# Performance work log

Measured on AMD Instinct MI355X. Metric: run time of the kernel, lower is better.

The kernel has to match this reference:

```python
import jax, jax.numpy as jnp
import numpy as np

B, N, DIN, DMID, DOUT, E = 64, 5000, 64, 128, 32, 80000


def setup_inputs() -> dict:
    key = jax.random.key(0)
    ks = jax.random.split(key, 12)
    p = lambda k, shape: jax.random.normal(k, shape, jnp.float32) * 0.05
    return {
        "x": jax.random.normal(ks[0], (B, N, DIN), jnp.float32),
        "edge_index": jax.random.randint(ks[1], (2, E), 0, N),
        "prev_hidden_state": jax.random.normal(ks[2], (B, N, DMID), jnp.float32),
        # GCNConv weights/biases for gates z, r, h
        "Wg_z": p(ks[3], (DIN, DMID)), "bg_z": jnp.zeros((DMID,), jnp.float32),
        "Wg_r": p(ks[4], (DIN, DMID)), "bg_r": jnp.zeros((DMID,), jnp.float32),
        "Wg_h": p(ks[5], (DIN, DMID)), "bg_h": jnp.zeros((DMID,), jnp.float32),
        # gate Linear layers on concat([conv_out, H]) -> DMID
        "Wl_z": p(ks[6], (2 * DMID, DMID)), "bl_z": jnp.zeros((DMID,), jnp.float32),
        "Wl_r": p(ks[7], (2 * DMID, DMID)), "bl_r": jnp.zeros((DMID,), jnp.float32),
        "Wl_h": p(ks[8], (2 * DMID, DMID)), "bl_h": jnp.zeros((DMID,), jnp.float32),
        # final output Linear
        "W_out": p(ks[9], (DMID, DOUT)), "b_out": jnp.zeros((DOUT,), jnp.float32),
    }


def reference(x, edge_index, prev_hidden_state,
              Wg_z, bg_z, Wg_r, bg_r, Wg_h, bg_h,
              Wl_z, bl_z, Wl_r, bl_r, Wl_h, bl_h,
              W_out, b_out):
    # GCN symmetric normalization with self-loops (pyg gcn_norm, improved=False)
    row, col = edge_index[0], edge_index[1]
    loop = jnp.arange(N)
    src = jnp.concatenate([row, loop])          # [E+N]
    dst = jnp.concatenate([col, loop])          # [E+N]
    ew = jnp.ones((E + N,), x.dtype)
    deg = jnp.zeros((N,), x.dtype).at[dst].add(ew)
    dis = jnp.where(deg > 0, jax.lax.rsqrt(jnp.maximum(deg, 1e-12)), 0.0)
    norm = dis[src] * ew * dis[dst]             # [E+N]

    def gcn(w, b):
        xw = jnp.einsum('bnd,de->bne', x, w)            # [B,N,DMID]
        msg = xw[:, src, :] * norm[None, :, None]       # gather + weight
        out = jnp.zeros((B, N, w.shape[1]), x.dtype).at[:, dst, :].add(msg)
        return out + b

    H = prev_hidden_state
    Z = jax.nn.sigmoid(jnp.concatenate([gcn(Wg_z, bg_z), H], -1) @ Wl_z + bl_z)
    R = jax.nn.sigmoid(jnp.concatenate([gcn(Wg_r, bg_r), H], -1) @ Wl_r + bl_r)
    Ht = jnp.tanh(jnp.concatenate([gcn(Wg_h, bg_h), H * R], -1) @ Wl_h + bl_h)
    H_new = Z * H + (1.0 - Z) * Ht                      # [B,N,DMID]

    y = jnp.mean(H_new, axis=1)                         # MeanAggregation over nodes
    y = jax.nn.relu(y) @ W_out + b_out                  # [B,DOUT]
    return (y, H_new)
```

## Files before the change

### kernel.cpp

```cpp
#include <hip/hip_runtime.h>
#include <cmath>

namespace {

constexpr int B = 64, N = 5000, DIN = 64, DMID = 128, DOUT = 32, E = 80000;
constexpr int NT = (N + 63) / 64;

typedef unsigned short u16;
typedef __attribute__((ext_vector_type(8))) short short8;
typedef __attribute__((ext_vector_type(4))) float floatx4;

#define MFMA16(a, b, c) __builtin_amdgcn_mfma_f32_16x16x32_bf16((a), (b), (c), 0, 0, 0)

__device__ __forceinline__ u16 f2bf(float f) {
  union { float f; unsigned u; } v; v.f = f;
  unsigned r = v.u + 0x7FFFu + ((v.u >> 16) & 1u);
  return (u16)(r >> 16);
}
__device__ __forceinline__ float bf2f(u16 s) {
  union { unsigned u; float f; } v; v.u = ((unsigned)s) << 16;
  return v.f;
}
__device__ __forceinline__ float sigmoid_fast(float x) {
  return __builtin_amdgcn_rcpf(1.f + __expf(-x));
}
__device__ __forceinline__ float tanh_fast(float x) {
  return fmaf(2.f, __builtin_amdgcn_rcpf(1.f + __expf(-2.f * x)), -1.f);
}


__global__ void count_kernel(const int* __restrict__ ei, int* counts) {
  int e = blockIdx.x * 256 + threadIdx.x;
  if (e < E) atomicAdd(&counts[ei[E + e]], 1);
}

__global__ void scan_kernel(int* counts, int* rowptr, float* dis) {
  __shared__ int sdata[1024];
  const int tid = threadIdx.x;
  constexpr int CH = (N + 1023) / 1024;
  int local[CH], cnt[CH];
  int s = 0;
  for (int i = 0; i < CH; i++) {
    int idx = tid * CH + i;
    int c = (idx < N) ? counts[idx] : 0;
    cnt[i] = c;
    local[i] = s;
    s += c;
  }
  sdata[tid] = s;
  __syncthreads();
  for (int off = 1; off < 1024; off <<= 1) {
    int v = (tid >= off) ? sdata[tid - off] : 0;
    __syncthreads();
    sdata[tid] += v;
    __syncthreads();
  }
  int prev = (tid > 0) ? sdata[tid - 1] : 0;
  for (int i = 0; i < CH; i++) {
    int idx = tid * CH + i;
    if (idx < N) {
      rowptr[idx] = prev + local[i];
      dis[idx] = rsqrtf((float)(cnt[i] + 1));
      counts[idx] = 0;
    }
  }
  if (tid == 1023) rowptr[N] = sdata[1023];
}

__global__ void fill_kernel(const int* __restrict__ ei, const int* __restrict__ rowptr,
                            const float* __restrict__ dis, int* counts,
                            int* csr_src, float* csr_w) {
  int e = blockIdx.x * 256 + threadIdx.x;
  if (e >= E) return;
  int r = ei[e], c = ei[E + e];
  int pos = rowptr[c] + atomicAdd(&counts[c], 1);
  csr_src[pos] = r;
  csr_w[pos] = dis[r] * dis[c];
}


__global__ void pack_kernel(const float* Wgz, const float* Wgr, const float* Wgh,
                            const float* Wlz, const float* Wlr, const float* Wlh,
                            const float* bgz, const float* bgr, const float* bgh,
                            const float* blz, const float* blr, const float* blh,
                            u16* wcB, u16* whB, float* bcAll) {
  int t = blockIdx.x * 256 + threadIdx.x;
  const float* Wg[3] = {Wgz, Wgr, Wgh};
  const float* Wl[3] = {Wlz, Wlr, Wlh};
  const float* bg[3] = {bgz, bgr, bgh};
  const float* bl[3] = {blz, blr, blh};
  if (t < 48 * 64) {
    int chunk = t >> 6, lane = t & 63;
    int q = lane >> 4, lm = lane & 15;
    int g = chunk >> 4, rem = chunk & 15, kt = rem >> 3, nt = rem & 7;
    int n = nt * 16 + lm;
#pragma unroll
    for (int jj = 0; jj < 8; jj++) {
      int k = kt * 32 + q * 8 + jj;
      float acc = 0.f;
      for (int j = 0; j < DMID; j++)
        acc = fmaf(Wg[g][k * DMID + j], Wl[g][j * DMID + n], acc);
      wcB[(size_t)(chunk * 64 + lane) * 8 + jj] = f2bf(acc);
    }
  } else if (t < 48 * 64 + 96 * 64) {
    int t2 = t - 48 * 64;
    int chunk = t2 >> 6, lane = t2 & 63;
    int q = lane >> 4, lm = lane & 15;
    int g = chunk >> 5, rem = chunk & 31, kt = rem >> 3, nt = rem & 7;
    int n = nt * 16 + lm;
#pragma unroll
    for (int jj = 0; jj < 8; jj++) {
      int k = kt * 32 + q * 8 + jj;
      whB[(size_t)t2 * 8 + jj] = f2bf(Wl[g][(DMID + k) * DMID + n]);
    }
  } else {
    int t3 = t - 48 * 64 - 96 * 64;
    if (t3 < 384) {
      int g = t3 >> 7, n = t3 & 127;
      float acc = bl[g][n];
      for (int j = 0; j < DMID; j++)
        acc = fmaf(bg[g][j], Wl[g][j * DMID + n], acc);
      bcAll[t3] = acc;
    }
  }
}


__global__ __launch_bounds__(256) void agg_kernel(
    const float* __restrict__ x, const int* __restrict__ rowptr,
    const int* __restrict__ csr_src, const float* __restrict__ csr_w,
    const float* __restrict__ dis, u16* __restrict__ xs) {
  constexpr int G = B * N / 16;
  const int bid = blockIdx.x;
  const int nb = (bid & 7) * (G >> 3) + (bid >> 3);
  const int sub = threadIdx.x >> 4;
  const int l16 = threadIdx.x & 15;
  const int unit = nb * 16 + sub;
  const int b = unit / N;
  const int n = unit - b * N;
  const float* xb = x + (size_t)b * N * DIN;
  const float d = dis[n];
  float4 v = *(const float4*)(xb + (size_t)n * DIN + l16 * 4);
  const float sw = d * d;
  float ax = v.x * sw, ay = v.y * sw, az = v.z * sw, aw = v.w * sw;
  const int s1 = rowptr[n + 1];
  int p = rowptr[n];
  for (; p + 4 <= s1; p += 4) {
    int i0 = csr_src[p], i1 = csr_src[p + 1], i2 = csr_src[p + 2], i3 = csr_src[p + 3];
    float w0 = csr_w[p], w1 = csr_w[p + 1], w2 = csr_w[p + 2], w3 = csr_w[p + 3];
    float4 a0 = *(const float4*)(xb + (size_t)i0 * DIN + l16 * 4);
    float4 a1 = *(const float4*)(xb + (size_t)i1 * DIN + l16 * 4);
    float4 a2 = *(const float4*)(xb + (size_t)i2 * DIN + l16 * 4);
    float4 a3 = *(const float4*)(xb + (size_t)i3 * DIN + l16 * 4);
    ax = fmaf(a0.x, w0, ax); ay = fmaf(a0.y, w0, ay);
    az = fmaf(a0.z, w0, az); aw = fmaf(a0.w, w0, aw);
    ax = fmaf(a1.x, w1, ax); ay = fmaf(a1.y, w1, ay);
    az = fmaf(a1.z, w1, az); aw = fmaf(a1.w, w1, aw);
    ax = fmaf(a2.x, w2, ax); ay = fmaf(a2.y, w2, ay);
    az = fmaf(a2.z, w2, az); aw = fmaf(a2.w, w2, aw);
    ax = fmaf(a3.x, w3, ax); ay = fmaf(a3.y, w3, ay);
    az = fmaf(a3.z, w3, az); aw = fmaf(a3.w, w3, aw);
  }
  for (; p < s1; p++) {
    int i0 = csr_src[p];
    float w0 = csr_w[p];
    float4 a0 = *(const float4*)(xb + (size_t)i0 * DIN + l16 * 4);
    ax = fmaf(a0.x, w0, ax); ay = fmaf(a0.y, w0, ay);
    az = fmaf(a0.z, w0, az); aw = fmaf(a0.w, w0, aw);
  }
  uint2 o;
  o.x = (unsigned)f2bf(ax) | ((unsigned)f2bf(ay) << 16);
  o.y = (unsigned)f2bf(az) | ((unsigned)f2bf(aw) << 16);
  *(uint2*)(xs + (size_t)unit * DIN + l16 * 4) = o;
}


constexpr int SH = 136;

__global__ __launch_bounds__(256, 4) void fused_mfma(
    const u16* __restrict__ xs, const float* __restrict__ H,
    const u16* __restrict__ wcB, const u16* __restrict__ whB,
    const float* __restrict__ bcAll,
    float* __restrict__ hnew, float* __restrict__ partials) {
  __shared__ u16 H_s[64 * SH];

  const int tid = threadIdx.x;
  const int b = blockIdx.y;
  const int n0 = blockIdx.x * 64;
  const int lane = tid & 63, w = tid >> 6;
  const int q = lane >> 4, lm = lane & 15;
  const int w16 = w * 16;

#pragma unroll
  for (int j = 0; j < 8; j++) {
    int idx = j * 64 + lane;
    int rl = idx >> 5, seg = idx & 31;
    int row = w16 + rl;
    float4 v = make_float4(0.f, 0.f, 0.f, 0.f);
    if (n0 + row < N) v = *(const float4*)(H + ((size_t)b * N + n0 + row) * DMID + seg * 4);
    uint2 p;
    p.x = (unsigned)f2bf(v.x) | ((unsigned)f2bf(v.y) << 16);
    p.y = (unsigned)f2bf(v.z) | ((unsigned)f2bf(v.w) << 16);
    *(uint2*)&H_s[row * SH + seg * 4] = p;
  }

  const int an = n0 + w16 + lm;
  short8 ax[2];
  if (an < N) {
    const u16* xrow = xs + ((size_t)b * N + an) * DIN;
    ax[0] = *(const short8*)(xrow + q * 8);
    ax[1] = *(const short8*)(xrow + 32 + q * 8);
  } else {
    ax[0] = short8{0, 0, 0, 0, 0, 0, 0, 0};
    ax[1] = short8{0, 0, 0, 0, 0, 0, 0, 0};
  }

  short8 ah[4];
#pragma unroll
  for (int kt = 0; kt < 4; kt++)
    ah[kt] = *(const short8*)&H_s[(w16 + lm) * SH + kt * 32 + q * 8];

  uint2 hstash[8];
#pragma unroll
  for (int nt = 0; nt < 8; nt++) {
    floatx4 a = {0.f, 0.f, 0.f, 0.f};
#pragma unroll
    for (int kt = 0; kt < 2; kt++)
      a = MFMA16(ax[kt], *(const short8*)(wcB + (size_t)((16 + kt * 8 + nt) * 64 + lane) * 8), a);
#pragma unroll
    for (int kt = 0; kt < 4; kt++)
      a = MFMA16(ah[kt], *(const short8*)(whB + (size_t)((32 + kt * 8 + nt) * 64 + lane) * 8), a);
    float bias = bcAll[128 + nt * 16 + lm];
    unsigned hx = 0u, hy = 0u;
#pragma unroll
    for (int r = 0; r < 4; r++) {
      int row = w16 + q * 4 + r, col = nt * 16 + lm;
      u16 hb = H_s[row * SH + col];
      float h = bf2f(hb);
      float rg = sigmoid_fast(a[r] + bias);
      H_s[row * SH + col] = f2bf(h * rg);
      if (r < 2) hx |= ((unsigned)hb) << (16 * r);
      else       hy |= ((unsigned)hb) << (16 * (r - 2));
    }
    hstash[nt] = make_uint2(hx, hy);
  }

  floatx4 zpre[8];
#pragma unroll
  for (int nt = 0; nt < 8; nt++) {
    floatx4 a = {0.f, 0.f, 0.f, 0.f};
#pragma unroll
    for (int kt = 0; kt < 2; kt++)
      a = MFMA16(ax[kt], *(const short8*)(wcB + (size_t)((0 + kt * 8 + nt) * 64 + lane) * 8), a);
#pragma unroll
    for (int kt = 0; kt < 4; kt++)
      a = MFMA16(ah[kt], *(const short8*)(whB + (size_t)((0 + kt * 8 + nt) * 64 + lane) * 8), a);
    zpre[nt] = a;
  }

  short8 ahr[4];
#pragma unroll
  for (int kt = 0; kt < 4; kt++)
    ahr[kt] = *(const short8*)&H_s[(w16 + lm) * SH + kt * 32 + q * 8];

#pragma unroll
  for (int nt = 0; nt < 8; nt++) {
    floatx4 ha = {0.f, 0.f, 0.f, 0.f};
#pragma unroll
    for (int kt = 0; kt < 2; kt++)
      ha = MFMA16(ax[kt], *(const short8*)(wcB + (size_t)((32 + kt * 8 + nt) * 64 + lane) * 8), ha);
#pragma unroll
    for (int kt = 0; kt < 4; kt++)
      ha = MFMA16(ahr[kt], *(const short8*)(whB + (size_t)((64 + kt * 8 + nt) * 64 + lane) * 8), ha);
    float zb = bcAll[nt * 16 + lm], hb_ = bcAll[256 + nt * 16 + lm];
    float colsum = 0.f;
#pragma unroll
    for (int r = 0; r < 4; r++) {
      int row = w16 + q * 4 + r;
      bool valid = (n0 + row) < N;
      unsigned word = (r < 2) ? hstash[nt].x : hstash[nt].y;
      float h = bf2f((u16)(word >> (16 * (r & 1))));
      float z = sigmoid_fast(zpre[nt][r] + zb);
      float ht = tanh_fast(ha[r] + hb_);
      float hn = fmaf(z, h - ht, ht);
      if (valid) {
        hnew[((size_t)b * N + n0 + row) * DMID + nt * 16 + lm] = hn;
        colsum += hn;
      }
    }
    colsum += __shfl_xor(colsum, 16);
    colsum += __shfl_xor(colsum, 32);
    if (lane < 16)
      partials[(((size_t)b * NT + blockIdx.x) * 4 + w) * DMID + nt * 16 + lane] = colsum;
  }
}


__global__ void out_kernel(const float* __restrict__ partials, const float* __restrict__ Wout,
                           const float* __restrict__ bout, float* __restrict__ y) {
  const int b = blockIdx.x;
  const int c = threadIdx.x;
  __shared__ float m[DMID];
  float acc = 0.f;
  for (int t = 0; t < NT * 4; t++)
    acc += partials[((size_t)b * NT * 4 + t) * DMID + c];
  m[c] = fmaxf(acc * (1.f / (float)N), 0.f);
  __syncthreads();
  if (c < DOUT) {
    float a2 = bout[c];
    for (int jj = 0; jj < DMID; jj++)
      a2 = fmaf(m[jj], Wout[jj * DOUT + c], a2);
    y[b * DOUT + c] = a2;
  }
}

}

extern "C" void kernel_launch(void* const* d_in, const int* in_sizes, int n_in,
                              void* d_out, int out_size, void* d_ws, size_t ws_size,
                              hipStream_t stream) {
  const float* x = (const float*)d_in[0];
  const int* ei = (const int*)d_in[1];
  const float* H = (const float*)d_in[2];
  const float* Wgz = (const float*)d_in[3];
  const float* bgz = (const float*)d_in[4];
  const float* Wgr = (const float*)d_in[5];
  const float* bgr = (const float*)d_in[6];
  const float* Wgh = (const float*)d_in[7];
  const float* bgh = (const float*)d_in[8];
  const float* Wlz = (const float*)d_in[9];
  const float* blz = (const float*)d_in[10];
  const float* Wlr = (const float*)d_in[11];
  const float* blr = (const float*)d_in[12];
  const float* Wlh = (const float*)d_in[13];
  const float* blh = (const float*)d_in[14];
  const float* Wout = (const float*)d_in[15];
  const float* bout = (const float*)d_in[16];

  float* y = (float*)d_out;
  float* hnew = (float*)d_out + (size_t)B * DOUT;

  char* p = (char*)d_ws;
  auto carve = [&](size_t bytes) {
    char* q = p;
    p += (bytes + 255) & ~size_t(255);
    return q;
  };
  int* counts = (int*)carve((size_t)N * 4);
  int* rowptr = (int*)carve((size_t)(N + 1) * 4);
  int* csr_src = (int*)carve((size_t)E * 4);
  float* csr_w = (float*)carve((size_t)E * 4);
  float* dis = (float*)carve((size_t)N * 4);
  u16* wcB = (u16*)carve((size_t)48 * 64 * 8 * 2);
  u16* whB = (u16*)carve((size_t)96 * 64 * 8 * 2);
  float* bcAll = (float*)carve((size_t)384 * 4);
  float* partials = (float*)carve((size_t)B * NT * 4 * DMID * 4);
  u16* xs = (u16*)carve((size_t)B * N * DIN * 2);

  hipMemsetAsync(counts, 0, (size_t)N * 4, stream);
  pack_kernel<<<38, 256, 0, stream>>>(Wgz, Wgr, Wgh, Wlz, Wlr, Wlh,
                                      bgz, bgr, bgh, blz, blr, blh,
                                      wcB, whB, bcAll);
  count_kernel<<<(E + 255) / 256, 256, 0, stream>>>(ei, counts);
  scan_kernel<<<1, 1024, 0, stream>>>(counts, rowptr, dis);
  fill_kernel<<<(E + 255) / 256, 256, 0, stream>>>(ei, rowptr, dis, counts, csr_src, csr_w);
  agg_kernel<<<B * N / 16, 256, 0, stream>>>(x, rowptr, csr_src, csr_w, dis, xs);
  fused_mfma<<<dim3(NT, B), 256, 0, stream>>>(xs, H, wcB, whB, bcAll, hnew, partials);
  out_kernel<<<B, DMID, 0, stream>>>(partials, Wout, bout, y);
}
```

Measured before the change: 734.4 us.

## Remap aggregation to one block per node across all batches; relax fused launch bounds

```diff
diff --git a/kernel.cpp b/kernel.cpp
--- a/kernel.cpp
+++ b/kernel.cpp
@@ -130,54 +130,75 @@
     const float* __restrict__ x, const int* __restrict__ rowptr,
     const int* __restrict__ csr_src, const float* __restrict__ csr_w,
     const float* __restrict__ dis, u16* __restrict__ xs) {
-  constexpr int G = B * N / 16;
-  const int bid = blockIdx.x;
-  const int nb = (bid & 7) * (G >> 3) + (bid >> 3);
-  const int sub = threadIdx.x >> 4;
-  const int l16 = threadIdx.x & 15;
-  const int unit = nb * 16 + sub;
-  const int b = unit / N;
-  const int n = unit - b * N;
-  const float* xb = x + (size_t)b * N * DIN;
+  const int n = blockIdx.x;
+  const int tb = threadIdx.x >> 2;
+  const int dq = threadIdx.x & 3;
+  const float* xbase = x + (size_t)tb * N * DIN + dq * 16;
+
   const float d = dis[n];
-  float4 v = *(const float4*)(xb + (size_t)n * DIN + l16 * 4);
   const float sw = d * d;
-  float ax = v.x * sw, ay = v.y * sw, az = v.z * sw, aw = v.w * sw;
+  float4 acc[4];
+  {
+    const float4* sp = (const float4*)(xbase + (size_t)n * DIN);
+#pragma unroll
+    for (int i = 0; i < 4; i++) {
+      float4 v = sp[i];
+      acc[i].x = v.x * sw; acc[i].y = v.y * sw;
+      acc[i].z = v.z * sw; acc[i].w = v.w * sw;
+    }
+  }
   const int s1 = rowptr[n + 1];
   int p = rowptr[n];
-  for (; p + 4 <= s1; p += 4) {
-    int i0 = csr_src[p], i1 = csr_src[p + 1], i2 = csr_src[p + 2], i3 = csr_src[p + 3];
-    float w0 = csr_w[p], w1 = csr_w[p + 1], w2 = csr_w[p + 2], w3 = csr_w[p + 3];
-    float4 a0 = *(const float4*)(xb + (size_t)i0 * DIN + l16 * 4);
-    float4 a1 = *(const float4*)(xb + (size_t)i1 * DIN + l16 * 4);
-    float4 a2 = *(const float4*)(xb + (size_t)i2 * DIN + l16 * 4);
-    float4 a3 = *(const float4*)(xb + (size_t)i3 * DIN + l16 * 4);
-    ax = fmaf(a0.x, w0, ax); ay = fmaf(a0.y, w0, ay);
-    az = fmaf(a0.z, w0, az); aw = fmaf(a0.w, w0, aw);
-    ax = fmaf(a1.x, w1, ax); ay = fmaf(a1.y, w1, ay);
-    az = fmaf(a1.z, w1, az); aw = fmaf(a1.w, w1, aw);
-    ax = fmaf(a2.x, w2, ax); ay = fmaf(a2.y, w2, ay);
-    az = fmaf(a2.z, w2, az); aw = fmaf(a2.w, w2, aw);
-    ax = fmaf(a3.x, w3, ax); ay = fmaf(a3.y, w3, ay);
-    az = fmaf(a3.z, w3, az); aw = fmaf(a3.w, w3, aw);
-  }
-  for (; p < s1; p++) {
+  for (; p + 2 <= s1; p += 2) {
+    int i0 = csr_src[p], i1 = csr_src[p + 1];
+    float w0 = csr_w[p], w1 = csr_w[p + 1];
+    const float4* s0p = (const float4*)(xbase + (size_t)i0 * DIN);
+    const float4* s1p = (const float4*)(xbase + (size_t)i1 * DIN);
+    float4 a0[4], a1[4];
+#pragma unroll
+    for (int i = 0; i < 4; i++) a0[i] = s0p[i];
+#pragma unroll
+    for (int i = 0; i < 4; i++) a1[i] = s1p[i];
+#pragma unroll
+    for (int i = 0; i < 4; i++) {
+      acc[i].x = fmaf(a0[i].x, w0, acc[i].x); acc[i].y = fmaf(a0[i].y, w0, acc[i].y);
+      acc[i].z = fmaf(a0[i].z, w0, acc[i].z); acc[i].w = fmaf(a0[i].w, w0, acc[i].w);
+    }
+#pragma unroll
+    for (int i = 0; i < 4; i++) {
+      acc[i].x = fmaf(a1[i].x, w1, acc[i].x); acc[i].y = fmaf(a1[i].y, w1, acc[i].y);
+      acc[i].z = fmaf(a1[i].z, w1, acc[i].z); acc[i].w = fmaf(a1[i].w, w1, acc[i].w);
+    }
+  }
+  if (p < s1) {
     int i0 = csr_src[p];
     float w0 = csr_w[p];
-    float4 a0 = *(const float4*)(xb + (size_t)i0 * DIN + l16 * 4);
-    ax = fmaf(a0.x, w0, ax); ay = fmaf(a0.y, w0, ay);
-    az = fmaf(a0.z, w0, az); aw = fmaf(a0.w, w0, aw);
-  }
-  uint2 o;
-  o.x = (unsigned)f2bf(ax) | ((unsigned)f2bf(ay) << 16);
-  o.y = (unsigned)f2bf(az) | ((unsigned)f2bf(aw) << 16);
-  *(uint2*)(xs + (size_t)unit * DIN + l16 * 4) = o;
+    const float4* s0p = (const float4*)(xbase + (size_t)i0 * DIN);
+#pragma unroll
+    for (int i = 0; i < 4; i++) {
+      float4 v = s0p[i];
+      acc[i].x = fmaf(v.x, w0, acc[i].x); acc[i].y = fmaf(v.y, w0, acc[i].y);
+      acc[i].z = fmaf(v.z, w0, acc[i].z); acc[i].w = fmaf(v.w, w0, acc[i].w);
+    }
+  }
+  uint4 o0, o1;
+  o0.x = (unsigned)f2bf(acc[0].x) | ((unsigned)f2bf(acc[0].y) << 16);
+  o0.y = (unsigned)f2bf(acc[0].z) | ((unsigned)f2bf(acc[0].w) << 16);
+  o0.z = (unsigned)f2bf(acc[1].x) | ((unsigned)f2bf(acc[1].y) << 16);
+  o0.w = (unsigned)f2bf(acc[1].z) | ((unsigned)f2bf(acc[1].w) << 16);
+  o1.x = (unsigned)f2bf(acc[2].x) | ((unsigned)f2bf(acc[2].y) << 16);
+  o1.y = (unsigned)f2bf(acc[2].z) | ((unsigned)f2bf(acc[2].w) << 16);
+  o1.z = (unsigned)f2bf(acc[3].x) | ((unsigned)f2bf(acc[3].y) << 16);
+  o1.w = (unsigned)f2bf(acc[3].z) | ((unsigned)f2bf(acc[3].w) << 16);
+  u16* out = xs + ((size_t)tb * N + n) * DIN + dq * 16;
+  *(uint4*)out = o0;
+  *(uint4*)(out + 8) = o1;
 }
 
 
 constexpr int SH = 136;
 
-__global__ __launch_bounds__(256, 4) void fused_mfma(
+__global__ __launch_bounds__(256, 3) void fused_mfma(
     const u16* __restrict__ xs, const float* __restrict__ H,
     const u16* __restrict__ wcB, const u16* __restrict__ whB,
     const float* __restrict__ bcAll,
@@ -364,7 +385,7 @@
   count_kernel<<<(E + 255) / 256, 256, 0, stream>>>(ei, counts);
   scan_kernel<<<1, 1024, 0, stream>>>(counts, rowptr, dis);
   fill_kernel<<<(E + 255) / 256, 256, 0, stream>>>(ei, rowptr, dis, counts, csr_src, csr_w);
-  agg_kernel<<<B * N / 16, 256, 0, stream>>>(x, rowptr, csr_src, csr_w, dis, xs);
+  agg_kernel<<<N, 256, 0, stream>>>(x, rowptr, csr_src, csr_w, dis, xs);
   fused_mfma<<<dim3(NT, B), 256, 0, stream>>>(xs, H, wcB, whB, bcAll, hnew, partials);
   out_kernel<<<B, DMID, 0, stream>>>(partials, Wout, bout, y);
 }
```

Measured after the change: 814.1 us. +10.9%, slower.
